# Kernel optimization log

Measured on AMD Instinct MI355X. Metric: run time of the kernel, lower is better.

## Reference

```python
import jax, jax.numpy as jnp
import numpy as np


def setup_inputs() -> dict:
    key = jax.random.key(0)
    k1, = jax.random.split(key, 1)
    B, H, W, C = 16, 64, 64, 256
    x = jax.random.normal(k1, (B, H, W, C), dtype=jnp.float32)
    gamma = jnp.zeros((1,), dtype=jnp.float32)
    return {"x": x, "gamma": gamma}


def reference(x, gamma):
    B, H, W, C = x.shape
    a = x.reshape(B, H * W, C)                      # [B, HW, C]
    # aTa[b, i, j] = sum_n a[b, n, i] * a[b, n, j]  -> [B, C, C]
    aTa = jnp.einsum('bni,bnj->bij', a, a)
    attn = jax.nn.softmax(aTa, axis=-1)             # softmax over last channel axis
    # aaTa[b, n, j] = sum_i a[b, n, i] * attn[b, i, j]
    aaTa = jnp.einsum('bni,bij->bnj', a, attn)      # [B, HW, C]
    aaTa = aaTa.reshape(B, H, W, C)
    return gamma * aaTa + x
```

## Files before the change

### kernel.cpp

```cpp
#include <hip/hip_runtime.h>
#include <hip/hip_bf16.h>


#define BB 16
#define NN 4096
#define CC 256
#define SPLITK 8
#define KCHUNK (NN / SPLITK)

typedef __attribute__((ext_vector_type(4))) short short4v;
typedef __attribute__((ext_vector_type(8))) short short8v;
typedef __attribute__((ext_vector_type(4))) float floatx4;

__device__ __forceinline__ unsigned short f2bf(float f) {
    unsigned int u = __float_as_uint(f);
    u += 0x7fffu + ((u >> 16) & 1u);
    return (unsigned short)(u >> 16);
}
__device__ __forceinline__ short4v cvt4(floatx4 v) {
    short4v r;
    r[0] = (short)f2bf(v[0]); r[1] = (short)f2bf(v[1]);
    r[2] = (short)f2bf(v[2]); r[3] = (short)f2bf(v[3]);
    return r;
}

__global__ __launch_bounds__(512, 2) void k_gemm1(const float* __restrict__ x,
                                                  float* __restrict__ part) {
    __shared__ unsigned short P[256 * 72];
    const int split = blockIdx.x;
    const int b     = blockIdx.y;
    const int half  = blockIdx.z;
    const int t  = threadIdx.x;
    const int w  = t >> 6, l = t & 63;
    const int lk = (l >> 4) * 8;
    const int lm = l & 15;
    const int i0 = half * 128;
    const int wr = (w >> 2) * 64;
    const int wc = (w & 3) * 64;
    const unsigned swz = (unsigned)(l & 7) << 3;

    const float* xb = x + ((size_t)b * NN + (size_t)split * KCHUNK) * CC + 4 * l;

    floatx4 pf[8];
    #pragma unroll
    for (int p = 0; p < 8; ++p)
        pf[p] = *(const floatx4*)(xb + (size_t)(w + 8 * p) * CC);

    floatx4 acc[4][4] = {};

    for (int k0 = 0; k0 < KCHUNK; k0 += 64) {
        short4v s[8];
        #pragma unroll
        for (int p = 0; p < 8; ++p) s[p] = cvt4(pf[p]);
        #pragma unroll
        for (int j = 0; j < 4; ++j) {
            short8v o;
            #pragma unroll
            for (int e = 0; e < 8; ++e) o[e] = s[e][j];
            const unsigned c = (unsigned)(4 * l + j);
            *(short8v*)&P[c * 72 + (((unsigned)(8 * w)) ^ swz)] = o;
        }
        __syncthreads();
        if (k0 + 64 < KCHUNK) {
            const float* xn = xb + (size_t)(k0 + 64) * CC;
            #pragma unroll
            for (int p = 0; p < 8; ++p)
                pf[p] = *(const floatx4*)(xn + (size_t)(w + 8 * p) * CC);
        }
        #pragma unroll
        for (int ks = 0; ks < 64; ks += 32) {
            short8v af[4], bf[4];
            #pragma unroll
            for (int mt = 0; mt < 4; ++mt) {
                const unsigned row = (unsigned)(i0 + wr + mt * 16 + lm);
                af[mt] = *(const short8v*)&P[row * 72 + (((unsigned)(ks + lk)) ^ (((row >> 2) & 7u) << 3))];
            }
            #pragma unroll
            for (int nt = 0; nt < 4; ++nt) {
                const unsigned row = (unsigned)(wc + nt * 16 + lm);
                bf[nt] = *(const short8v*)&P[row * 72 + (((unsigned)(ks + lk)) ^ (((row >> 2) & 7u) << 3))];
            }
            #pragma unroll
            for (int mt = 0; mt < 4; ++mt)
                #pragma unroll
                for (int nt = 0; nt < 4; ++nt)
                    acc[mt][nt] = __builtin_amdgcn_mfma_f32_16x16x32_bf16(af[mt], bf[nt], acc[mt][nt], 0, 0, 0);
        }
        __syncthreads();
    }
    const int orow = (l >> 4) * 4;
    float* pout = part + (size_t)(split * BB + b) * CC * CC;
    #pragma unroll
    for (int mt = 0; mt < 4; ++mt)
        #pragma unroll
        for (int nt = 0; nt < 4; ++nt)
            #pragma unroll
            for (int r = 0; r < 4; ++r) {
                int i = i0 + wr + mt * 16 + orow + r;
                int j = wc + nt * 16 + lm;
                pout[(size_t)i * CC + j] = acc[mt][nt][r];
            }
}

__global__ __launch_bounds__(256) void k_softmax(const float* __restrict__ part,
                                                 unsigned short* __restrict__ attnT) {
    const int w = threadIdx.x >> 6;
    const int l = threadIdx.x & 63;
    const int row = blockIdx.x * 4 + w;
    const int b = row >> 8;
    const int i = row & 255;
    float v0 = 0.f, v1 = 0.f, v2 = 0.f, v3 = 0.f;
    #pragma unroll
    for (int s = 0; s < SPLITK; ++s) {
        const float* p = part + ((size_t)(s * BB + b) * CC + i) * CC;
        v0 += p[l]; v1 += p[l + 64]; v2 += p[l + 128]; v3 += p[l + 192];
    }
    float m = fmaxf(fmaxf(v0, v1), fmaxf(v2, v3));
    for (int off = 32; off >= 1; off >>= 1) m = fmaxf(m, __shfl_xor(m, off, 64));
    v0 = __expf(v0 - m); v1 = __expf(v1 - m); v2 = __expf(v2 - m); v3 = __expf(v3 - m);
    float s = v0 + v1 + v2 + v3;
    for (int off = 32; off >= 1; off >>= 1) s += __shfl_xor(s, off, 64);
    float rs = 1.0f / s;
    unsigned short* o = attnT + (size_t)b * CC * CC + i;
    o[(size_t)(l +   0) * CC] = f2bf(v0 * rs);
    o[(size_t)(l +  64) * CC] = f2bf(v1 * rs);
    o[(size_t)(l + 128) * CC] = f2bf(v2 * rs);
    o[(size_t)(l + 192) * CC] = f2bf(v3 * rs);
}

__global__ __launch_bounds__(256) void k_gemm2(const float* __restrict__ x,
                                               const unsigned short* __restrict__ attnT,
                                               const float* __restrict__ gamma,
                                               float* __restrict__ out) {
    __shared__ unsigned short At[64 * 72];
    __shared__ unsigned short Bt[256 * 72];
    const int n0 = blockIdx.x * 64;
    const int b  = blockIdx.y;
    const int t  = threadIdx.x;
    const int w  = t >> 6, l = t & 63;
    const int lk = (l >> 4) * 8, lm = l & 15;
    const int sc = t >> 4, sk = (t & 15) * 4;

    const float*          Abase = x + ((size_t)b * NN + n0) * CC;
    const unsigned short* Bbase = attnT + (size_t)b * CC * CC;

    floatx4 acc[4][4] = {};
    for (int k0 = 0; k0 < CC; k0 += 64) {
        #pragma unroll
        for (int r = 0; r < 4; ++r) {
            int n = sc + 16 * r;
            floatx4 av = *(const floatx4*)(Abase + (size_t)n * CC + k0 + sk);
            *(short4v*)&At[n * 72 + sk] = cvt4(av);
        }
        #pragma unroll
        for (int r = 0; r < 16; ++r) {
            int j = sc + 16 * r;
            *(short4v*)&Bt[j * 72 + sk] = *(const short4v*)(Bbase + (size_t)j * CC + k0 + sk);
        }
        __syncthreads();
        #pragma unroll
        for (int ks = 0; ks < 64; ks += 32) {
            short8v af[4], bf[4];
            #pragma unroll
            for (int mt = 0; mt < 4; ++mt)
                af[mt] = *(const short8v*)&At[(mt * 16 + lm) * 72 + ks + lk];
            #pragma unroll
            for (int nt = 0; nt < 4; ++nt)
                bf[nt] = *(const short8v*)&Bt[(w * 64 + nt * 16 + lm) * 72 + ks + lk];
            #pragma unroll
            for (int mt = 0; mt < 4; ++mt)
                #pragma unroll
                for (int nt = 0; nt < 4; ++nt)
                    acc[mt][nt] = __builtin_amdgcn_mfma_f32_16x16x32_bf16(af[mt], bf[nt], acc[mt][nt], 0, 0, 0);
        }
        __syncthreads();
    }
    const float g = gamma[0];
    const int orow = (l >> 4) * 4;
    #pragma unroll
    for (int mt = 0; mt < 4; ++mt)
        #pragma unroll
        for (int nt = 0; nt < 4; ++nt)
            #pragma unroll
            for (int r = 0; r < 4; ++r) {
                int nr = n0 + mt * 16 + orow + r;
                int j  = w * 64 + nt * 16 + lm;
                size_t idx = ((size_t)b * NN + nr) * CC + j;
                out[idx] = g * acc[mt][nt][r] + x[idx];
            }
}

extern "C" void kernel_launch(void* const* d_in, const int* in_sizes, int n_in,
                              void* d_out, int out_size, void* d_ws, size_t ws_size,
                              hipStream_t stream) {
    const float* x     = (const float*)d_in[0];
    const float* gamma = (const float*)d_in[1];
    float* out = (float*)d_out;

    char* ws = (char*)d_ws;
    float*          part  = (float*)ws;
    unsigned short* attnT = (unsigned short*)(ws + (size_t)SPLITK * BB * CC * CC * 4);

    k_gemm1  <<<dim3(SPLITK, BB, 2),  512, 0, stream>>>(x, part);
    k_softmax<<<dim3(BB * CC / 4),    256, 0, stream>>>(part, attnT);
    k_gemm2  <<<dim3(NN / 64, BB),    256, 0, stream>>>(x, attnT, gamma, out);
}
```

Baseline: 159.8 us.

## Deepen global-load prefetch in both GEMMs and use LDS-only barriers

In k_gemm1 the global prefetch is double-buffered, with two register sets loaded two steps ahead, so loads stay in flight across the barrier. k_gemm2 gains register prefetch of the next A/B tiles before its compute phase and an occupancy hint of 3 blocks per CU. __syncthreads is replaced by an asm barrier that waits only on LDS counters, so outstanding global loads are not drained. This raises register pressure, which could cause spills or lower occupancy, and relies on the inline-asm barrier being correct.

```diff
diff --git a/kernel.cpp b/kernel.cpp
--- a/kernel.cpp
+++ b/kernel.cpp
@@ -22,6 +22,9 @@
     r[0] = (short)f2bf(v[0]); r[1] = (short)f2bf(v[1]);
     r[2] = (short)f2bf(v[2]); r[3] = (short)f2bf(v[3]);
     return r;
+}
+__device__ __forceinline__ void lds_barrier() {
+    asm volatile("s_waitcnt lgkmcnt(0)\n\ts_barrier" ::: "memory");
 }
 
 __global__ __launch_bounds__(512, 2) void k_gemm1(const float* __restrict__ x,
@@ -41,17 +44,19 @@
 
     const float* xb = x + ((size_t)b * NN + (size_t)split * KCHUNK) * CC + 4 * l;
 
-    floatx4 pf[8];
-    #pragma unroll
-    for (int p = 0; p < 8; ++p)
-        pf[p] = *(const floatx4*)(xb + (size_t)(w + 8 * p) * CC);
-
     floatx4 acc[4][4] = {};
 
-    for (int k0 = 0; k0 < KCHUNK; k0 += 64) {
+    auto LOADP = [&](floatx4 (&pf)[8], int k0) {
+        const float* xn = xb + (size_t)k0 * CC;
+        #pragma unroll
+        for (int p = 0; p < 8; ++p)
+            pf[p] = *(const floatx4*)(xn + (size_t)(w + 8 * p) * CC);
+    };
+    auto STEP = [&](floatx4 (&pf)[8], int k0) {
         short4v s[8];
         #pragma unroll
         for (int p = 0; p < 8; ++p) s[p] = cvt4(pf[p]);
+        if (k0 + 128 < KCHUNK) LOADP(pf, k0 + 128);
         #pragma unroll
         for (int j = 0; j < 4; ++j) {
             short8v o;
@@ -60,13 +65,7 @@
             const unsigned c = (unsigned)(4 * l + j);
             *(short8v*)&P[c * 72 + (((unsigned)(8 * w)) ^ swz)] = o;
         }
-        __syncthreads();
-        if (k0 + 64 < KCHUNK) {
-            const float* xn = xb + (size_t)(k0 + 64) * CC;
-            #pragma unroll
-            for (int p = 0; p < 8; ++p)
-                pf[p] = *(const floatx4*)(xn + (size_t)(w + 8 * p) * CC);
-        }
+        lds_barrier();
         #pragma unroll
         for (int ks = 0; ks < 64; ks += 32) {
             short8v af[4], bf[4];
@@ -86,8 +85,18 @@
                 for (int nt = 0; nt < 4; ++nt)
                     acc[mt][nt] = __builtin_amdgcn_mfma_f32_16x16x32_bf16(af[mt], bf[nt], acc[mt][nt], 0, 0, 0);
         }
-        __syncthreads();
+        lds_barrier();
+    };
+
+    floatx4 pfA[8], pfB[8];
+    LOADP(pfA, 0);
+    LOADP(pfB, 64);
+    #pragma unroll
+    for (int k0 = 0; k0 < KCHUNK; k0 += 128) {
+        STEP(pfA, k0);
+        STEP(pfB, k0 + 64);
     }
+
     const int orow = (l >> 4) * 4;
     float* pout = part + (size_t)(split * BB + b) * CC * CC;
     #pragma unroll
@@ -128,10 +137,10 @@
     o[(size_t)(l + 192) * CC] = f2bf(v3 * rs);
 }
 
-__global__ __launch_bounds__(256) void k_gemm2(const float* __restrict__ x,
-                                               const unsigned short* __restrict__ attnT,
-                                               const float* __restrict__ gamma,
-                                               float* __restrict__ out) {
+__global__ __launch_bounds__(256, 3) void k_gemm2(const float* __restrict__ x,
+                                                  const unsigned short* __restrict__ attnT,
+                                                  const float* __restrict__ gamma,
+                                                  float* __restrict__ out) {
     __shared__ unsigned short At[64 * 72];
     __shared__ unsigned short Bt[256 * 72];
     const int n0 = blockIdx.x * 64;
@@ -144,20 +153,31 @@
     const float*          Abase = x + ((size_t)b * NN + n0) * CC;
     const unsigned short* Bbase = attnT + (size_t)b * CC * CC;
 
+    floatx4 pA[4];
+    short4v pB[16];
+    auto LOADA = [&](int k0) {
+        #pragma unroll
+        for (int r = 0; r < 4; ++r)
+            pA[r] = *(const floatx4*)(Abase + (size_t)(sc + 16 * r) * CC + k0 + sk);
+    };
+    auto LOADB = [&](int k0) {
+        #pragma unroll
+        for (int r = 0; r < 16; ++r)
+            pB[r] = *(const short4v*)(Bbase + (size_t)(sc + 16 * r) * CC + k0 + sk);
+    };
+
     floatx4 acc[4][4] = {};
+    LOADA(0); LOADB(0);
+    #pragma unroll
     for (int k0 = 0; k0 < CC; k0 += 64) {
         #pragma unroll
-        for (int r = 0; r < 4; ++r) {
-            int n = sc + 16 * r;
-            floatx4 av = *(const floatx4*)(Abase + (size_t)n * CC + k0 + sk);
-            *(short4v*)&At[n * 72 + sk] = cvt4(av);
-        }
-        #pragma unroll
-        for (int r = 0; r < 16; ++r) {
-            int j = sc + 16 * r;
-            *(short4v*)&Bt[j * 72 + sk] = *(const short4v*)(Bbase + (size_t)j * CC + k0 + sk);
-        }
-        __syncthreads();
+        for (int r = 0; r < 4; ++r)
+            *(short4v*)&At[(sc + 16 * r) * 72 + sk] = cvt4(pA[r]);
+        #pragma unroll
+        for (int r = 0; r < 16; ++r)
+            *(short4v*)&Bt[(sc + 16 * r) * 72 + sk] = pB[r];
+        if (k0 + 64 < CC) { LOADA(k0 + 64); LOADB(k0 + 64); }
+        lds_barrier();
         #pragma unroll
         for (int ks = 0; ks < 64; ks += 32) {
             short8v af[4], bf[4];
@@ -173,7 +193,7 @@
                 for (int nt = 0; nt < 4; ++nt)
                     acc[mt][nt] = __builtin_amdgcn_mfma_f32_16x16x32_bf16(af[mt], bf[nt], acc[mt][nt], 0, 0, 0);
         }
-        __syncthreads();
+        lds_barrier();
     }
     const float g = gamma[0];
     const int orow = (l >> 4) * 4;
```

Result: slower. 209.7 us (+31.2%).

## Restructure gemm2: stage full A row-tile once, read B from global, vectorize epilogue

Applied to the files above, without the earlier changes.

The second GEMM now loads the whole 64x256 activation tile into LDS once, with a single barrier, instead of staging A and B per 64-wide k-step behind two barriers each. The bf16 attention operand is read straight from global/L2 into registers, and the k-loop is fully unrolled. The epilogue uses a 4x4 lane transpose via shuffles so each lane does 16-byte loads of x and 16-byte stores of out instead of scalar accesses. This trades LDS reuse of B for fewer synchronizations and wider output accesses, and launch bounds now request 4 blocks per CU.

```diff
diff --git a/kernel.cpp b/kernel.cpp
--- a/kernel.cpp
+++ b/kernel.cpp
@@ -128,66 +128,70 @@
     o[(size_t)(l + 192) * CC] = f2bf(v3 * rs);
 }
 
-__global__ __launch_bounds__(256) void k_gemm2(const float* __restrict__ x,
-                                               const unsigned short* __restrict__ attnT,
-                                               const float* __restrict__ gamma,
-                                               float* __restrict__ out) {
-    __shared__ unsigned short At[64 * 72];
-    __shared__ unsigned short Bt[256 * 72];
+#define ALD 260
+__global__ __launch_bounds__(256, 4) void k_gemm2(const float* __restrict__ x,
+                                                  const unsigned short* __restrict__ attnT,
+                                                  const float* __restrict__ gamma,
+                                                  float* __restrict__ out) {
+    __shared__ unsigned short At[64 * ALD];
     const int n0 = blockIdx.x * 64;
     const int b  = blockIdx.y;
     const int t  = threadIdx.x;
     const int w  = t >> 6, l = t & 63;
     const int lk = (l >> 4) * 8, lm = l & 15;
-    const int sc = t >> 4, sk = (t & 15) * 4;
-
-    const float*          Abase = x + ((size_t)b * NN + n0) * CC;
-    const unsigned short* Bbase = attnT + (size_t)b * CC * CC;
-
+
+    const float* Abase = x + ((size_t)b * NN + n0) * CC;
+
+    #pragma unroll
+    for (int r = 0; r < 16; ++r) {
+        int idx = r * 256 + t;
+        int row = idx >> 6;
+        int col = (idx & 63) * 4;
+        floatx4 v = *(const floatx4*)(Abase + (size_t)row * CC + col);
+        *(short4v*)&At[row * ALD + col] = cvt4(v);
+    }
+    __syncthreads();
+
+    const unsigned short* Bb = attnT + (size_t)b * CC * CC;
     floatx4 acc[4][4] = {};
-    for (int k0 = 0; k0 < CC; k0 += 64) {
-        #pragma unroll
-        for (int r = 0; r < 4; ++r) {
-            int n = sc + 16 * r;
-            floatx4 av = *(const floatx4*)(Abase + (size_t)n * CC + k0 + sk);
-            *(short4v*)&At[n * 72 + sk] = cvt4(av);
-        }
-        #pragma unroll
-        for (int r = 0; r < 16; ++r) {
-            int j = sc + 16 * r;
-            *(short4v*)&Bt[j * 72 + sk] = *(const short4v*)(Bbase + (size_t)j * CC + k0 + sk);
-        }
-        __syncthreads();
-        #pragma unroll
-        for (int ks = 0; ks < 64; ks += 32) {
-            short8v af[4], bf[4];
-            #pragma unroll
-            for (int mt = 0; mt < 4; ++mt)
-                af[mt] = *(const short8v*)&At[(mt * 16 + lm) * 72 + ks + lk];
+    #pragma unroll
+    for (int k0 = 0; k0 < CC; k0 += 32) {
+        short8v af[4], bf[4];
+        #pragma unroll
+        for (int mt = 0; mt < 4; ++mt)
+            af[mt] = *(const short8v*)&At[(mt * 16 + lm) * ALD + k0 + lk];
+        #pragma unroll
+        for (int nt = 0; nt < 4; ++nt)
+            bf[nt] = *(const short8v*)(Bb + (size_t)(w * 64 + nt * 16 + lm) * CC + k0 + lk);
+        #pragma unroll
+        for (int mt = 0; mt < 4; ++mt)
             #pragma unroll
             for (int nt = 0; nt < 4; ++nt)
-                bf[nt] = *(const short8v*)&Bt[(w * 64 + nt * 16 + lm) * 72 + ks + lk];
-            #pragma unroll
-            for (int mt = 0; mt < 4; ++mt)
-                #pragma unroll
-                for (int nt = 0; nt < 4; ++nt)
-                    acc[mt][nt] = __builtin_amdgcn_mfma_f32_16x16x32_bf16(af[mt], bf[nt], acc[mt][nt], 0, 0, 0);
-        }
-        __syncthreads();
-    }
+                acc[mt][nt] = __builtin_amdgcn_mfma_f32_16x16x32_bf16(af[mt], bf[nt], acc[mt][nt], 0, 0, 0);
+    }
+
     const float g = gamma[0];
     const int orow = (l >> 4) * 4;
     #pragma unroll
     for (int mt = 0; mt < 4; ++mt)
         #pragma unroll
-        for (int nt = 0; nt < 4; ++nt)
-            #pragma unroll
-            for (int r = 0; r < 4; ++r) {
-                int nr = n0 + mt * 16 + orow + r;
-                int j  = w * 64 + nt * 16 + lm;
-                size_t idx = ((size_t)b * NN + nr) * CC + j;
-                out[idx] = g * acc[mt][nt][r] + x[idx];
-            }
+        for (int nt = 0; nt < 4; ++nt) {
+            float v0 = acc[mt][nt][0], v1 = acc[mt][nt][1];
+            float v2 = acc[mt][nt][2], v3 = acc[mt][nt][3];
+            float tt;
+            tt = __shfl_xor((lm & 1) ? v0 : v1, 1, 64); if (lm & 1) v0 = tt; else v1 = tt;
+            tt = __shfl_xor((lm & 1) ? v2 : v3, 1, 64); if (lm & 1) v2 = tt; else v3 = tt;
+            tt = __shfl_xor((lm & 2) ? v0 : v2, 2, 64); if (lm & 2) v0 = tt; else v2 = tt;
+            tt = __shfl_xor((lm & 2) ? v1 : v3, 2, 64); if (lm & 2) v1 = tt; else v3 = tt;
+            int nr = n0 + mt * 16 + orow + (lm & 3);
+            int jc = w * 64 + nt * 16 + (lm & 12);
+            size_t ro = ((size_t)b * NN + nr) * CC + jc;
+            floatx4 xv = *(const floatx4*)(x + ro);
+            floatx4 ov;
+            ov[0] = g * v0 + xv[0]; ov[1] = g * v1 + xv[1];
+            ov[2] = g * v2 + xv[2]; ov[3] = g * v3 + xv[3];
+            *(floatx4*)(out + ro) = ov;
+        }
 }
 
 extern "C" void kernel_launch(void* const* d_in, const int* in_sizes, int n_in,
```

After: 165.7 us. +3.7%, slower.
